# Optimization experiments

Hardware: AMD Instinct MI355X
Metric: run time of the kernel (lower is better)

Reference implementation:

```python
import jax, jax.numpy as jnp
import numpy as np
import math

# D4 group multiplication permutations (rows of the 8x8 regular representation)
PERMS = (
    (0, 1, 2, 3, 4, 5, 6, 7),
    (3, 0, 1, 2, 5, 6, 7, 4),
    (2, 3, 0, 1, 6, 7, 4, 5),
    (1, 2, 3, 0, 7, 4, 5, 6),
    (4, 5, 6, 7, 0, 1, 2, 3),
    (5, 6, 7, 4, 3, 0, 1, 2),
    (6, 7, 4, 5, 2, 3, 0, 1),
    (7, 4, 5, 6, 1, 2, 3, 0),
)


def d4_1x1(x, w):
    """D4-equivariant 1x1 conv. x: (b, cin*8, h, w), w: (cout, cin, 8)."""
    b, C, h, ww = x.shape
    cout, cin, _ = w.shape
    # (cout, 8, cin, 8): permuted copies of the base weight
    W = jnp.stack([w[..., jnp.array(p)] for p in PERMS], axis=1)
    xr = x.reshape(b, cin, 8, h, ww)
    y = jnp.einsum('ogif,bifhw->boghw', W, xr)
    return y.reshape(b, cout * 8, h, ww)


def group_norm(x, gamma, beta, num_groups, eps=1e-5):
    b, C, h, w = x.shape
    xg = x.reshape(b, num_groups, C // num_groups, h, w)
    mean = xg.mean(axis=(2, 3, 4), keepdims=True)
    var = xg.var(axis=(2, 3, 4), keepdims=True)
    xn = ((xg - mean) / jnp.sqrt(var + eps)).reshape(b, C, h, w)
    return xn * gamma[None, :, None, None] + beta[None, :, None, None]


def unfold_patches(x, k):
    """torch.nn.Unfold(k, 1, (k-1)//2, 1) -> (b, C, k*k, h, w), patch idx = ki*k+kj."""
    b, C, h, w = x.shape
    p = (k - 1) // 2
    xp = jnp.pad(x, ((0, 0), (0, 0), (p, p), (p, p)))
    pats = jnp.stack([xp[:, :, i:i + h, j:j + w]
                      for i in range(k) for j in range(k)], axis=2)
    return pats


def setup_inputs() -> dict:
    key = jax.random.key(0)
    ks = jax.random.split(key, 4)
    b, H, W = 8, 56, 56
    cin, cout, rr, k, gc = 64, 64, 2, 3, 16
    cmid = cin // rr            # 32
    G = cout // gc              # 4 dynamic-kernel groups
    x = jax.random.normal(ks[0], (b, cin * 8, H, W), jnp.float32)
    w_v = jax.random.normal(ks[1], (cout, cin, 8), jnp.float32) / math.sqrt(8 * cin / 2)
    w1 = jax.random.normal(ks[2], (cmid, cin, 8), jnp.float32) / math.sqrt(8 * cin / 2)
    gn_gamma = jnp.ones((cmid * 8,), jnp.float32)
    gn_beta = jnp.zeros((cmid * 8,), jnp.float32)
    w2 = jax.random.normal(ks[3], (k * k * G, cmid), jnp.float32) / math.sqrt(cmid)
    b2 = jnp.zeros((k * k * G,), jnp.float32)
    return {"x": x, "w_v": w_v, "w1": w1, "gn_gamma": gn_gamma,
            "gn_beta": gn_beta, "w2": w2, "b2": b2}


def reference(x, w_v, w1, gn_gamma, gn_beta, w2, b2):
    k, gc = 3, 16
    b, _, h, w = x.shape
    cmid = w1.shape[0]
    G = w2.shape[0] // (k * k)
    # --- dynamic kernel branch: conv1 (D4 1x1 + GN + ReLU), conv2 (1x1x1 conv3d)
    t = jax.nn.relu(group_norm(d4_1x1(x, w1), gn_gamma, gn_beta, cmid))
    tr = t.reshape(b, cmid, 8, h, w)
    wgt = jnp.einsum('oi,bighw->boghw', w2, tr) + b2[None, :, None, None, None]
    wv = wgt.reshape(b, G, k, k, 8, h, w)
    # --- D4 symmetrization of the k x k kernel per group element
    s = [wv[:, :, :, :, g] for g in range(8)]          # each (b,G,k,k,h,w)
    sw = [jnp.swapaxes(s[g], 2, 3) for g in range(4, 8)]
    trans = [s[0],
             jnp.rot90(s[1], 1, (2, 3)),
             jnp.rot90(s[2], 2, (2, 3)),
             jnp.rot90(s[3], 3, (2, 3)),
             jnp.rot90(sw[0], 3, (2, 3)),
             jnp.rot90(sw[1], 2, (2, 3)),
             jnp.rot90(sw[2], 1, (2, 3)),
             sw[3]]
    wv = jnp.stack(trans, axis=4)                      # (b,G,k,k,8,h,w)
    wv = wv.reshape(b, G, k * k, 8, h, w)[:, :, None]  # (b,G,1,k^2,8,h,w)
    wv = jnp.swapaxes(wv, 3, 4)                        # (b,G,1,8,k^2,h,w)
    # --- value branch + unfold + multiply-sum
    xv = d4_1x1(x, w_v)                                # (b, cout*8, h, w)
    pats = unfold_patches(xv, k).reshape(b, G, gc, 8, k * k, h, w)
    out = (wv * pats).sum(axis=4)                      # (b,G,gc,8,h,w)
    return out.reshape(b, G * gc * 8, h, w)
```

## Files before the change

### kernel.cpp

```cpp
#include <hip/hip_runtime.h>

#define BATCH 8
#define PIX   3136
#define CIN8  512
#define CMID8 256
#define KDIM  512

typedef short short8 __attribute__((ext_vector_type(8)));
typedef float f32x4 __attribute__((ext_vector_type(4)));

__constant__ int c_perms[8][8] = {
    {0, 1, 2, 3, 4, 5, 6, 7},
    {3, 0, 1, 2, 5, 6, 7, 4},
    {2, 3, 0, 1, 6, 7, 4, 5},
    {1, 2, 3, 0, 7, 4, 5, 6},
    {4, 5, 6, 7, 0, 1, 2, 3},
    {5, 6, 7, 4, 3, 0, 1, 2},
    {6, 7, 4, 5, 2, 3, 0, 1},
};
__constant__ int c_perm7[8] = {7, 4, 5, 6, 1, 2, 3, 0};

__constant__ int c_tab[8][9] = {
    {0, 1, 2, 3, 4, 5, 6, 7, 8},
    {2, 5, 8, 1, 4, 7, 0, 3, 6},
    {8, 7, 6, 5, 4, 3, 2, 1, 0},
    {6, 3, 0, 7, 4, 1, 8, 5, 2},
    {2, 1, 0, 5, 4, 3, 8, 7, 6},
    {8, 5, 2, 7, 4, 1, 6, 3, 0},
    {6, 7, 8, 3, 4, 5, 0, 1, 2},
    {0, 3, 6, 1, 4, 7, 2, 5, 8},
};

__device__ __forceinline__ float bf2f(unsigned short u) {
    union { unsigned int i; float f; } v;
    v.i = ((unsigned int)u) << 16;
    return v.f;
}
__device__ __forceinline__ unsigned short f2bf(float f) {
    union { float f; unsigned int u; } v;
    v.f = f;
    unsigned int u = v.u;
    u += 0x7FFFu + ((u >> 16) & 1u);
    return (unsigned short)(u >> 16);
}
__device__ __forceinline__ float bflo(unsigned int u) {
    union { unsigned int i; float f; } v; v.i = u << 16; return v.f;
}
__device__ __forceinline__ float bfhi(unsigned int u) {
    union { unsigned int i; float f; } v; v.i = u & 0xFFFF0000u; return v.f;
}

__device__ __forceinline__ void gload_lds16(const unsigned short* g, unsigned short* l) {
    __builtin_amdgcn_global_load_lds(
        (const __attribute__((address_space(1))) unsigned int*)g,
        (__attribute__((address_space(3))) unsigned int*)l,
        16, 0, 0);
}

#define LDT 70
__global__ __launch_bounds__(256) void cvt_t_kernel(
    const float* __restrict__ x, unsigned short* __restrict__ xbfT)
{
    __shared__ unsigned short T[64 * LDT];
    const int flat = blockIdx.x;
    const int kt = flat & 7;
    const int pt = (flat >> 3) % 49;
    const int b  = flat / (49 * 8);
    const int k0 = kt * 64, p0 = pt * 64;

    const float* xb = x + ((size_t)b * CIN8 + k0) * PIX + p0;
    const int kl = threadIdx.x >> 4;
    const int pl = (threadIdx.x & 15) * 4;
#pragma unroll
    for (int pass = 0; pass < 4; ++pass) {
        int kk = kl + pass * 16;
        float4 v = *(const float4*)(xb + (size_t)kk * PIX + pl);
        ushort2 lo = {f2bf(v.x), f2bf(v.y)};
        ushort2 hi = {f2bf(v.z), f2bf(v.w)};
        *(ushort2*)&T[kk * LDT + pl]     = lo;
        *(ushort2*)&T[kk * LDT + pl + 2] = hi;
    }
    __syncthreads();
    const int prow = threadIdx.x >> 2;
    const int kc8  = (threadIdx.x & 3) * 8;
    unsigned short* ob = xbfT + ((size_t)b * PIX + p0 + prow) * KDIM + k0;
#pragma unroll
    for (int pass = 0; pass < 2; ++pass) {
        int kk = kc8 + pass * 32;
        unsigned short tmp[8];
#pragma unroll
        for (int j = 0; j < 8; ++j) tmp[j] = T[(kk + j) * LDT + prow];
        *(uint4*)(ob + kk) = *(const uint4*)tmp;
    }
}

__global__ __launch_bounds__(256) void build_w_kernel(
    const float* __restrict__ w_v, const float* __restrict__ w1,
    unsigned short* __restrict__ Wbig, float* __restrict__ stats2)
{
    if (blockIdx.x < 2) stats2[blockIdx.x * 256 + threadIdx.x] = 0.f;

    int idx = blockIdx.x * 256 + threadIdx.x;
    int r = idx >> 9;
    int k = idx & 511;
    int i = k >> 3, f = k & 7;
    float v;
    if (r < 512) {
        int o = r >> 3, g = r & 7;
        int pf = (g < 7) ? c_perms[g][f] : c_perm7[f];
        v = w_v[(o * 64 + i) * 8 + pf];
    } else {
        int rr = r - 512;
        int o = rr >> 3, g = rr & 7;
        int pf = (g < 7) ? c_perms[g][f] : c_perm7[f];
        v = w1[(o * 64 + i) * 8 + pf];
    }
    Wbig[idx] = f2bf(v);
}

__global__ __launch_bounds__(256) void gemm_kernel(
    const unsigned short* __restrict__ xT,
    const unsigned short* __restrict__ Wbig,
    unsigned short* __restrict__ xv,
    float* __restrict__ y1,
    float* __restrict__ stats2)
{
    __shared__ unsigned short Wt[2][128 * 64];
    __shared__ unsigned short Xt[2][128 * 64];

    const int swz = (blockIdx.x & 7) * 147 + (blockIdx.x >> 3);
    const int rt  = swz % 6;
    const int pt  = swz / 6;
    const int row0 = rt * 128;
    const int P0   = pt * 128;

    const int tid  = threadIdx.x;
    const int lane = tid & 63;
    const int wave = tid >> 6;
    const int wm   = wave & 1;
    const int wn   = wave >> 1;

    f32x4 acc[4][4];
#pragma unroll
    for (int i = 0; i < 4; ++i)
#pragma unroll
        for (int j = 0; j < 4; ++j) acc[i][j] = (f32x4){0.f, 0.f, 0.f, 0.f};

    const int lr  = lane >> 3;
    const int lc  = lane & 7;
    const int swc = ((lc ^ lr) * 8);
    const unsigned short* wsrc = Wbig + (size_t)(row0 + wave * 32 + lr) * KDIM + swc;
    const unsigned short* xsrc = xT + (size_t)(P0 + wave * 32 + lr) * KDIM + swc;
    const int wofs = (wave * 32) * 64;

    const int m16 = lane & 15;
    const int lq  = lane >> 4;
    const int swr = m16 & 7;

#define STAGE(buf, k0) do {                                                   \
    _Pragma("unroll")                                                         \
    for (int i = 0; i < 4; ++i) {                                             \
        gload_lds16(wsrc + (size_t)i * 8 * KDIM + (k0), &Wt[buf][wofs] + i * 512); \
        gload_lds16(xsrc + (size_t)i * 8 * KDIM + (k0), &Xt[buf][wofs] + i * 512); \
    }                                                                         \
} while (0)

    STAGE(0, 0);
    __syncthreads();

    int cur = 0;
    for (int kc = 0; kc < 8; ++kc) {
        if (kc < 7) STAGE(cur ^ 1, (kc + 1) * 64);

#pragma unroll
        for (int kk = 0; kk < 2; ++kk) {
            const int ck = (((kk << 2) | lq) ^ swr) * 8;
            short8 bfrag[4];
#pragma unroll
            for (int nt = 0; nt < 4; ++nt)
                bfrag[nt] = *(const short8*)&Xt[cur][(wn * 64 + nt * 16 + m16) * 64 + ck];
#pragma unroll
            for (int mt = 0; mt < 4; ++mt) {
                short8 afrag = *(const short8*)&Wt[cur][(wm * 64 + mt * 16 + m16) * 64 + ck];
#pragma unroll
                for (int nt = 0; nt < 4; ++nt)
                    acc[mt][nt] = __builtin_amdgcn_mfma_f32_16x16x32_bf16(
                        afrag, bfrag[nt], acc[mt][nt], 0, 0, 0);
            }
        }
        __syncthreads();
        cur ^= 1;
    }
#undef STAGE

    const int colw = P0 + wn * 64;
    const int bb   = colw / PIX;
    const int pq   = colw - bb * PIX;
    const int qm   = lq * 4;

    if (row0 < 512) {
        unsigned short* dst0 = xv + ((size_t)bb * CIN8) * PIX + pq + m16;
#pragma unroll
        for (int nt = 0; nt < 4; ++nt) {
            unsigned short* dst = dst0 + nt * 16;
#pragma unroll
            for (int mt = 0; mt < 4; ++mt) {
                const int m = row0 + wm * 64 + mt * 16 + qm;
#pragma unroll
                for (int r = 0; r < 4; ++r)
                    dst[(size_t)(m + r) * PIX] = f2bf(acc[mt][nt][r]);
            }
        }
    } else {
        float* dst0 = y1 + ((size_t)bb * CMID8) * PIX + pq + m16;
#pragma unroll
        for (int nt = 0; nt < 4; ++nt) {
            float* dst = dst0 + nt * 16;
#pragma unroll
            for (int mt = 0; mt < 4; ++mt) {
                const int m = (row0 - 512) + wm * 64 + mt * 16 + qm;
#pragma unroll
                for (int r = 0; r < 4; ++r)
                    dst[(size_t)(m + r) * PIX] = acc[mt][nt][r];
            }
        }
        const int gbase = ((row0 - 512) + wm * 64) >> 3;
#pragma unroll
        for (int mt = 0; mt < 4; ++mt) {
            float s = 0.f, ss = 0.f;
#pragma unroll
            for (int nt = 0; nt < 4; ++nt)
#pragma unroll
                for (int r = 0; r < 4; ++r) {
                    float v = acc[mt][nt][r];
                    s += v; ss += v * v;
                }
#pragma unroll
            for (int off = 1; off <= 16; off <<= 1) {
                s  += __shfl_xor(s, off);
                ss += __shfl_xor(ss, off);
            }
            if ((lane & 31) == 0) {
                const int g = gbase + 2 * mt + (lane >> 5);
                atomicAdd(&stats2[(bb * 32 + g) * 2],     s);
                atomicAdd(&stats2[(bb * 32 + g) * 2 + 1], ss);
            }
        }
    }
}

__global__ __launch_bounds__(256) void final_fused_kernel(
    const float* __restrict__ y1, const float* __restrict__ stats2,
    const float* __restrict__ gamma, const float* __restrict__ beta,
    const float* __restrict__ w2, const float* __restrict__ b2,
    const unsigned short* __restrict__ xv,
    float* __restrict__ out)
{
    const int swz  = (blockIdx.x & 7) * 128 + (blockIdx.x >> 3);
    const int combo = swz >> 2;
    const int b    = combo >> 5;
    const int g    = (combo >> 2) & 7;
    const int gidx = combo & 3;

    __shared__ float w2s[9 * 32];
    __shared__ float b2s9[9];
    __shared__ float scs[32], shs[32];
    const int tid = threadIdx.x;
    for (int i = tid; i < 288; i += 256) {
        int tt = i >> 5, ic = i & 31;
        w2s[i] = w2[(gidx * 9 + c_tab[g][tt]) * 32 + ic];
    }
    if (tid < 9) b2s9[tid] = b2[gidx * 9 + c_tab[g][tid]];
    if (tid < 32) {
        float S  = stats2[(b * 32 + tid) * 2];
        float SS = stats2[(b * 32 + tid) * 2 + 1];
        float mean = S * (1.f / 25088.f);
        float var  = SS * (1.f / 25088.f) - mean * mean;
        float rstd = rsqrtf(var + 1e-5f);
        float sc = rstd * gamma[tid * 8 + g];
        scs[tid] = sc;
        shs[tid] = beta[tid * 8 + g] - mean * sc;
    }
    __syncthreads();

    const int pp = (swz & 3) * 256 + tid;
    if (pp >= 784) return;
    const int p0 = pp * 4;
    const int h  = p0 / 56;
    const int w0 = p0 % 56;

    float wt[4][9];
#pragma unroll
    for (int i = 0; i < 4; ++i)
#pragma unroll
        for (int tt = 0; tt < 9; ++tt) wt[i][tt] = b2s9[tt];

    const float* yb = y1 + ((size_t)b * CMID8 + g) * PIX + p0;
#pragma unroll 4
    for (int ic = 0; ic < 32; ++ic) {
        float4 v = *(const float4*)(yb + (size_t)(ic * 8) * PIX);
        float t0 = v.x * scs[ic] + shs[ic]; t0 = t0 > 0.f ? t0 : 0.f;
        float t1 = v.y * scs[ic] + shs[ic]; t1 = t1 > 0.f ? t1 : 0.f;
        float t2 = v.z * scs[ic] + shs[ic]; t2 = t2 > 0.f ? t2 : 0.f;
        float t3 = v.w * scs[ic] + shs[ic]; t3 = t3 > 0.f ? t3 : 0.f;
#pragma unroll
        for (int tt = 0; tt < 9; ++tt) {
            float wv = w2s[tt * 32 + ic];
            wt[0][tt] = fmaf(wv, t0, wt[0][tt]);
            wt[1][tt] = fmaf(wv, t1, wt[1][tt]);
            wt[2][tt] = fmaf(wv, t2, wt[2][tt]);
            wt[3][tt] = fmaf(wv, t3, wt[3][tt]);
        }
    }

    int rb[3];
#pragma unroll
    for (int ki = 0; ki < 3; ++ki) {
        int hh = h + ki - 1;
        bool rv = (hh >= 0) & (hh < 56);
        int hc = hh < 0 ? 0 : (hh > 55 ? 55 : hh);
        rb[ki] = hc * 56;
        if (!rv) {
#pragma unroll
            for (int i = 0; i < 4; ++i)
#pragma unroll
                for (int kj = 0; kj < 3; ++kj) wt[i][ki * 3 + kj] = 0.f;
        }
    }
#pragma unroll
    for (int i = 0; i < 4; ++i)
#pragma unroll
        for (int tt = 0; tt < 9; ++tt) {
            int ww = w0 + i + (tt % 3) - 1;
            if (ww < 0 || ww >= 56) wt[i][tt] = 0.f;
        }

    const int c0 = (w0 == 0) ? 0 : (w0 - 2);

    const unsigned short* xc = xv + ((size_t)b * CIN8 + gidx * 128 + g) * PIX;
    float* ob = out + ((size_t)b * CIN8 + gidx * 128 + g) * PIX + p0;
#pragma unroll 2
    for (int cc = 0; cc < 16; ++cc) {
        f32x4 a = (f32x4){0.f, 0.f, 0.f, 0.f};
#pragma unroll
        for (int ki = 0; ki < 3; ++ki) {
            const unsigned short* row = xc + rb[ki];
            unsigned int u0 = *(const unsigned int*)(row + c0);
            unsigned int u1 = *(const unsigned int*)(row + w0);
            unsigned int u2 = *(const unsigned int*)(row + w0 + 2);
            unsigned int u3 = *(const unsigned int*)(row + w0 + 4);
            float f1 = bfhi(u0);
            float f2 = bflo(u1), f3 = bfhi(u1);
            float f4 = bflo(u2), f5 = bfhi(u2);
            float f6 = bflo(u3);
            const int t0i = ki * 3;
            a[0] = fmaf(wt[0][t0i + 0], f1, a[0]);
            a[0] = fmaf(wt[0][t0i + 1], f2, a[0]);
            a[0] = fmaf(wt[0][t0i + 2], f3, a[0]);
            a[1] = fmaf(wt[1][t0i + 0], f2, a[1]);
            a[1] = fmaf(wt[1][t0i + 1], f3, a[1]);
            a[1] = fmaf(wt[1][t0i + 2], f4, a[1]);
            a[2] = fmaf(wt[2][t0i + 0], f3, a[2]);
            a[2] = fmaf(wt[2][t0i + 1], f4, a[2]);
            a[2] = fmaf(wt[2][t0i + 2], f5, a[2]);
            a[3] = fmaf(wt[3][t0i + 0], f4, a[3]);
            a[3] = fmaf(wt[3][t0i + 1], f5, a[3]);
            a[3] = fmaf(wt[3][t0i + 2], f6, a[3]);
        }
        *(f32x4*)(ob + (size_t)cc * 8 * PIX) = a;
        xc += (size_t)8 * PIX;
    }
}

extern "C" void kernel_launch(void* const* d_in, const int* in_sizes, int n_in,
                              void* d_out, int out_size, void* d_ws, size_t ws_size,
                              hipStream_t stream) {
    (void)in_sizes; (void)n_in; (void)out_size; (void)ws_size;
    const float* x     = (const float*)d_in[0];
    const float* w_v   = (const float*)d_in[1];
    const float* w1    = (const float*)d_in[2];
    const float* gamma = (const float*)d_in[3];
    const float* beta  = (const float*)d_in[4];
    const float* w2    = (const float*)d_in[5];
    const float* b2    = (const float*)d_in[6];
    float* out = (float*)d_out;

    char* ws = (char*)d_ws;
    unsigned short* Wbig = (unsigned short*)ws;
    unsigned short* xbfT = (unsigned short*)(ws + 786432);
    unsigned short* xv   = (unsigned short*)(ws + 26476544);
    float* y1     = (float*)(ws + 52166656);
    float* stats2 = (float*)(ws + 77856768);

    cvt_t_kernel<<<3136, 256, 0, stream>>>(x, xbfT);
    build_w_kernel<<<1536, 256, 0, stream>>>(w_v, w1, Wbig, stats2);
    gemm_kernel<<<1176, 256, 0, stream>>>(xbfT, Wbig, xv, y1, stats2);
    final_fused_kernel<<<256 * 4, 256, 0, stream>>>(
        y1, stats2, gamma, beta, w2, b2, xv, out);
}
```

Before: 171.6 us.

## Halve GEMM K-tile and prefetch two stages ahead with explicit vmcnt waits

```diff
diff --git a/kernel.cpp b/kernel.cpp
--- a/kernel.cpp
+++ b/kernel.cpp
@@ -118,15 +118,15 @@
     Wbig[idx] = f2bf(v);
 }
 
-__global__ __launch_bounds__(256) void gemm_kernel(
+__global__ __launch_bounds__(256, 5) void gemm_kernel(
     const unsigned short* __restrict__ xT,
     const unsigned short* __restrict__ Wbig,
     unsigned short* __restrict__ xv,
     float* __restrict__ y1,
     float* __restrict__ stats2)
 {
-    __shared__ unsigned short Wt[2][128 * 64];
-    __shared__ unsigned short Xt[2][128 * 64];
+    __shared__ unsigned short Wt[2][128 * 32];
+    __shared__ unsigned short Xt[2][128 * 32];
 
     const int swz = (blockIdx.x & 7) * 147 + (blockIdx.x >> 3);
     const int rt  = swz % 6;
@@ -146,49 +146,53 @@
 #pragma unroll
         for (int j = 0; j < 4; ++j) acc[i][j] = (f32x4){0.f, 0.f, 0.f, 0.f};
 
-    const int lr  = lane >> 3;
-    const int lc  = lane & 7;
-    const int swc = ((lc ^ lr) * 8);
-    const unsigned short* wsrc = Wbig + (size_t)(row0 + wave * 32 + lr) * KDIM + swc;
-    const unsigned short* xsrc = xT + (size_t)(P0 + wave * 32 + lr) * KDIM + swc;
-    const int wofs = (wave * 32) * 64;
+    const int lr  = lane >> 2;
+    const int lc  = lane & 3;
+    const int qc0 = lc ^ ((lr >> 1) & 3);
+    const unsigned short* wsrc = Wbig + (size_t)(row0 + wave * 32 + lr) * KDIM + qc0 * 8;
+    const unsigned short* xsrc = xT + (size_t)(P0 + wave * 32 + lr) * KDIM + qc0 * 8;
+    const int wofs = wave * 1024;
 
     const int m16 = lane & 15;
     const int lq  = lane >> 4;
-    const int swr = m16 & 7;
-
-#define STAGE(buf, k0) do {                                                   \
-    _Pragma("unroll")                                                         \
-    for (int i = 0; i < 4; ++i) {                                             \
-        gload_lds16(wsrc + (size_t)i * 8 * KDIM + (k0), &Wt[buf][wofs] + i * 512); \
-        gload_lds16(xsrc + (size_t)i * 8 * KDIM + (k0), &Xt[buf][wofs] + i * 512); \
-    }                                                                         \
+    const int ckq = (lq ^ ((m16 >> 1) & 3)) * 8;
+
+#define STAGE(buf, kt) do {                                                     \
+    _Pragma("unroll")                                                           \
+    for (int i = 0; i < 2; ++i) {                                               \
+        gload_lds16(wsrc + (size_t)i * 16 * KDIM + (kt) * 32, &Wt[buf][wofs + i * 512]); \
+        gload_lds16(xsrc + (size_t)i * 16 * KDIM + (kt) * 32, &Xt[buf][wofs + i * 512]); \
+    }                                                                           \
 } while (0)
 
     STAGE(0, 0);
-    __syncthreads();
+    STAGE(1, 1);
+    asm volatile("s_waitcnt vmcnt(4)\n\ts_barrier" ::: "memory");
 
     int cur = 0;
-    for (int kc = 0; kc < 8; ++kc) {
-        if (kc < 7) STAGE(cur ^ 1, (kc + 1) * 64);
-
-#pragma unroll
-        for (int kk = 0; kk < 2; ++kk) {
-            const int ck = (((kk << 2) | lq) ^ swr) * 8;
-            short8 bfrag[4];
+#pragma unroll 2
+    for (int kc = 0; kc < 16; ++kc) {
+        short8 bfrag[4];
+#pragma unroll
+        for (int nt = 0; nt < 4; ++nt)
+            bfrag[nt] = *(const short8*)&Xt[cur][(wn * 64 + nt * 16 + m16) * 32 + ckq];
+#pragma unroll
+        for (int mt = 0; mt < 4; ++mt) {
+            short8 afrag = *(const short8*)&Wt[cur][(wm * 64 + mt * 16 + m16) * 32 + ckq];
 #pragma unroll
             for (int nt = 0; nt < 4; ++nt)
-                bfrag[nt] = *(const short8*)&Xt[cur][(wn * 64 + nt * 16 + m16) * 64 + ck];
-#pragma unroll
-            for (int mt = 0; mt < 4; ++mt) {
-                short8 afrag = *(const short8*)&Wt[cur][(wm * 64 + mt * 16 + m16) * 64 + ck];
-#pragma unroll
-                for (int nt = 0; nt < 4; ++nt)
-                    acc[mt][nt] = __builtin_amdgcn_mfma_f32_16x16x32_bf16(
-                        afrag, bfrag[nt], acc[mt][nt], 0, 0, 0);
-            }
-        }
-        __syncthreads();
+                acc[mt][nt] = __builtin_amdgcn_mfma_f32_16x16x32_bf16(
+                    afrag, bfrag[nt], acc[mt][nt], 0, 0, 0);
+        }
+        if (kc == 15) break;
+
+        asm volatile("s_barrier" ::: "memory");
+        if (kc < 14) {
+            STAGE(cur, kc + 2);
+            asm volatile("s_waitcnt vmcnt(4)\n\ts_barrier" ::: "memory");
+        } else {
+            asm volatile("s_waitcnt vmcnt(0)\n\ts_barrier" ::: "memory");
+        }
         cur ^= 1;
     }
 #undef STAGE
```

Result: slower. 187.8 us (+9.5%).
